# Kernel optimization log

Measured on AMD Instinct MI355X. Metric: run time of the kernel, lower is better.

## Reference

```python
import jax, jax.numpy as jnp
import numpy as np

B, S, F = 2048, 512, 64   # batch, seq_len, input_features
H = 32                    # LSTM_HIDDEN_SIZE
H1, H2 = 32, 16           # HIDDEN_SIZES
O = 3                     # output_features


def setup_inputs() -> dict:
    key = jax.random.key(0)
    ks = jax.random.split(key, 10)
    sc = lambda n: 1.0 / np.sqrt(n)
    x = jax.random.normal(ks[0], (B, S, F), dtype=jnp.float32)
    # LSTM kernels, gate order (i, f, g, o); input kernel has no bias (flax LSTMCell),
    # hidden kernel carries the bias.
    Wx = jax.random.normal(ks[1], (F, 4 * H), dtype=jnp.float32) * sc(F)
    Wh = jax.random.normal(ks[2], (H, 4 * H), dtype=jnp.float32) * sc(H)
    b = jnp.zeros((4 * H,), dtype=jnp.float32)
    # MLP head: 32 -> 32 -> 16 -> 3 with leaky_relu between hidden layers
    W1 = jax.random.normal(ks[3], (H, H1), dtype=jnp.float32) * sc(H)
    b1 = jnp.zeros((H1,), dtype=jnp.float32)
    W2 = jax.random.normal(ks[4], (H1, H2), dtype=jnp.float32) * sc(H1)
    b2 = jnp.zeros((H2,), dtype=jnp.float32)
    Wo = jax.random.normal(ks[5], (H2, O), dtype=jnp.float32) * sc(H2)
    bo = jnp.zeros((O,), dtype=jnp.float32)
    return {"x": x, "Wx": Wx, "Wh": Wh, "b": b,
            "W1": W1, "b1": b1, "W2": W2, "b2": b2, "Wo": Wo, "bo": bo}


def _lstm_last_hidden(x, Wx, Wh, b):
    # Precompute input-to-gate projections for all timesteps (same math,
    # hoists the [B,S,F]x[F,4H] GEMM out of the scan).
    bsz = x.shape[0]
    h_dim = Wh.shape[0]
    xg = jnp.einsum('bsf,fg->sbg', x, Wx)  # [S, B, 4H], time-major for scan

    def step(carry, xg_t):
        c, h = carry
        z = xg_t + h @ Wh + b               # [B, 4H]
        i, f, g, o = jnp.split(z, 4, axis=-1)
        i = jax.nn.sigmoid(i)
        f = jax.nn.sigmoid(f)
        g = jnp.tanh(g)
        o = jax.nn.sigmoid(o)
        c_new = f * c + i * g
        h_new = o * jnp.tanh(c_new)
        return (c_new, h_new), None

    c0 = jnp.zeros((bsz, h_dim), dtype=x.dtype)
    h0 = jnp.zeros((bsz, h_dim), dtype=x.dtype)
    (c_T, h_T), _ = jax.lax.scan(step, (c0, h0), xg)
    return h_T  # last hidden state, matches x[1][:, -1, :]


def reference(x, Wx, Wh, b, W1, b1, W2, b2, Wo, bo):
    h = _lstm_last_hidden(x, Wx, Wh, b)        # [B, H]
    a = jax.nn.leaky_relu(h @ W1 + b1)         # [B, 32]
    a = jax.nn.leaky_relu(a @ W2 + b2)         # [B, 16]
    return a @ Wo + bo                         # [B, O]
```

## Files before the change

kernel.cpp:

```cpp
#include <hip/hip_runtime.h>
#include <hip/hip_bf16.h>

#define S_  512
#define F_  64
#define H_  32
#define GQ  128
#define BT  8
#define NB  256

#define XS  72
#define HS  40
#define GS  33

#define L2E 1.4426950408889634f
#define CN2 (-2.8853900817779268f)

typedef __attribute__((ext_vector_type(8))) short bf16x8;
typedef __attribute__((ext_vector_type(4))) float f32x4;

__device__ __forceinline__ unsigned short bf16s(float f) {
    return __builtin_bit_cast(unsigned short, __float2bfloat16(f));
}
__device__ __forceinline__ unsigned bf16pk(float x, float y) {
    return (unsigned)bf16s(x) | ((unsigned)bf16s(y) << 16);
}
__device__ __forceinline__ float sigm2(float z) {
    return __builtin_amdgcn_rcpf(1.0f + __builtin_amdgcn_exp2f(-z));
}
__device__ __forceinline__ float tanh2(float c) {
    return 2.0f * __builtin_amdgcn_rcpf(1.0f + __builtin_amdgcn_exp2f(c * CN2)) - 1.0f;
}

#define MFMA(A, B, C) __builtin_amdgcn_mfma_f32_16x16x32_bf16(A, B, C, 0, 0, 0)

__global__ __launch_bounds__(512, 1)
void lstm_mfma_kernel(const float* __restrict__ x,  const float* __restrict__ Wx,
                      const float* __restrict__ Wh, const float* __restrict__ bg,
                      const float* __restrict__ W1, const float* __restrict__ b1,
                      const float* __restrict__ W2, const float* __restrict__ b2,
                      const float* __restrict__ Wo, const float* __restrict__ bo,
                      float* __restrict__ out)
{
    const int tid = threadIdx.x;
    const int w   = tid >> 6;
    const int L   = tid & 63;
    const int c16 = L & 15;
    const int kg  = L >> 4;
    const int bb  = blockIdx.x * BT;
    const int jj  = (w << 2) + kg;

    const int gcol = ((c16 & 3) << 5) + (w << 2) + (c16 >> 2);
    const float gsc = ((c16 & 3) == 2) ? (2.0f * L2E) : L2E;

    __shared__ __align__(16) unsigned short xh[4][16][XS];
    __shared__ __align__(16) unsigned short hh[2][16][HS];
    __shared__ float Hd[3][BT][GS];

    bf16x8 whh_, wx0h, wx1h;
#pragma unroll
    for (int i = 0; i < 8; ++i) {
        wx0h[i] = (short)bf16s(Wx[(kg * 8 + i) * GQ + gcol] * gsc);
        wx1h[i] = (short)bf16s(Wx[(32 + kg * 8 + i) * GQ + gcol] * gsc);
        whh_[i] = (short)bf16s(Wh[(kg * 8 + i) * GQ + gcol] * gsc);
    }
    f32x4 biasC;
#pragma unroll
    for (int r = 0; r < 4; ++r)
        biasC[r] = bg[r * 32 + jj] * ((r == 2) ? (2.0f * L2E) : L2E);

    for (int i = tid; i < 2 * 16 * (HS / 2); i += 512)
        ((unsigned*)&hh[0][0][0])[i] = 0u;

    const int srow = tid >> 5;
    const int sfp  = tid & 31;
    const int sdt  = srow >> 3;
    const float* xsrc = x + (size_t)(bb + (srow & 7)) * S_ * F_ + 2 * sfp;
    const float* xs2  = xsrc + (size_t)sdt * F_;
    {
#pragma unroll
        for (int tt = 0; tt < 2; ++tt) {
            float2 v = *(const float2*)(xs2 + (size_t)(2 * tt) * F_);
            *(unsigned*)&xh[tt][srow][2 * sfp] = bf16pk(v.x, v.y);
        }
    }
    float2 xvA = *(const float2*)(xs2 + (size_t)4 * F_);
    float2 xvB = *(const float2*)(xs2 + (size_t)6 * F_);
    __syncthreads();

    f32x4 xzA, xz1A, xzB, xz1B;
    {
        bf16x8 bxh0 = *(const bf16x8*)&xh[0][c16][kg * 8];
        bf16x8 bxh1 = *(const bf16x8*)&xh[0][c16][32 + kg * 8];
        f32x4 b0 = MFMA(wx0h, bxh0, biasC);
        xzA = MFMA(wx1h, bxh1, b0);
#pragma unroll
        for (int r = 0; r < 4; ++r) xz1A[r] = __shfl_xor(xzA[r], 8);
    }

    float cc = 0.0f;

#define DSTEP(TD, XZIN, XZ1IN, XZOUT, XZ1OUT, XV) {                            \
    const int td = (TD);                                                       \
         \
    *(unsigned*)&xh[(td + 2) & 3][srow][2 * sfp] = bf16pk(XV.x, XV.y);         \
    int tl = td + 4; if (tl > 255) tl = 255;                                   \
    XV = *(const float2*)(xs2 + (size_t)(2 * tl) * F_);                        \
    const int s1 = (td + 1) & 3;                                               \
           \
    bf16x8 bxh0 = *(const bf16x8*)&xh[s1][c16][kg * 8];                        \
    bf16x8 bhh1 = *(const bf16x8*)&hh[1][c16][kg * 8];                         \
    f32x4 part = MFMA(wx0h, bxh0, biasC);                                      \
    f32x4 z = MFMA(whh_, bhh1, XZIN);                                          \
    float iv = sigm2(z[0]), fv = sigm2(z[1]);                                  \
    float gv = 2.0f * sigm2(z[2]) - 1.0f, ov = sigm2(z[3]);                    \
    cc = fmaf(fv, cc, iv * gv);                                                \
    float hv = ov * tanh2(cc);                                                 \
    if (c16 < 8) hh[0][c16][jj] = bf16s(hv);                                   \
    __syncthreads();                                    \
                              \
    bf16x8 bxh1 = *(const bf16x8*)&xh[s1][c16][32 + kg * 8];                   \
    bf16x8 bhh0 = *(const bf16x8*)&hh[0][c16][kg * 8];                         \
    XZOUT = MFMA(wx1h, bxh1, part);                                            \
    _Pragma("unroll")                                                          \
    for (int r = 0; r < 4; ++r) XZ1OUT[r] = __shfl_xor(XZOUT[r], 8);           \
    z = MFMA(whh_, bhh0, XZ1IN);                                               \
    iv = sigm2(z[0]); fv = sigm2(z[1]);                                        \
    gv = 2.0f * sigm2(z[2]) - 1.0f; ov = sigm2(z[3]);                          \
    cc = fmaf(fv, cc, iv * gv);                                                \
    hv = ov * tanh2(cc);                                                       \
    if (c16 < 8) {                                                             \
        hh[1][c16][jj] = bf16s(hv);                                            \
        if (td == 255) Hd[0][c16][jj] = hv;                                    \
    }                                                                          \
    __syncthreads();                      \
}

    for (int qd = 0; qd < 128; ++qd) {
        DSTEP(2 * qd,     xzA, xz1A, xzB, xz1B, xvA)
        DSTEP(2 * qd + 1, xzB, xz1B, xzA, xz1A, xvB)
    }
#undef DSTEP

    __syncthreads();

    if (tid < 256) {
        int rb = tid >> 5, n = tid & 31;
        float a = b1[n];
#pragma unroll
        for (int k = 0; k < 32; ++k) a = fmaf(Hd[0][rb][k], W1[k * 32 + n], a);
        a = (a > 0.0f) ? a : 0.01f * a;
        Hd[1][rb][n] = a;
    }
    __syncthreads();
    if (tid < 128) {
        int rb = tid >> 4, n = tid & 15;
        float a = b2[n];
#pragma unroll
        for (int k = 0; k < 32; ++k) a = fmaf(Hd[1][rb][k], W2[k * 16 + n], a);
        a = (a > 0.0f) ? a : 0.01f * a;
        Hd[2][rb][n] = a;
    }
    __syncthreads();
    if (tid < 24) {
        int rb = tid / 3, n = tid - rb * 3;
        float a = bo[n];
#pragma unroll
        for (int k = 0; k < 16; ++k) a = fmaf(Hd[2][rb][k], Wo[k * 3 + n], a);
        out[(size_t)(bb + rb) * 3 + n] = a;
    }
}

extern "C" void kernel_launch(void* const* d_in, const int* in_sizes, int n_in,
                              void* d_out, int out_size, void* d_ws, size_t ws_size,
                              hipStream_t stream) {
    const float* x  = (const float*)d_in[0];
    const float* Wx = (const float*)d_in[1];
    const float* Wh = (const float*)d_in[2];
    const float* bg = (const float*)d_in[3];
    const float* W1 = (const float*)d_in[4];
    const float* b1 = (const float*)d_in[5];
    const float* W2 = (const float*)d_in[6];
    const float* b2 = (const float*)d_in[7];
    const float* Wo = (const float*)d_in[8];
    const float* bo = (const float*)d_in[9];
    float* out = (float*)d_out;

    hipLaunchKernelGGL(lstm_mfma_kernel, dim3(NB), dim3(512), 0, stream,
                       x, Wx, Wh, bg, W1, b1, W2, b2, Wo, bo, out);
}
```

Measured before the change: 139.4 us.

## Halve batch tile per block, run two blocks per CU, load x directly into registers

Each block now handles 4 batch rows instead of 8, doubling the block count, and launch bounds allow two blocks per CU so the latency-bound recurrence steps of two blocks can interleave. The LDS staging buffer for x is removed: each lane loads its own 8+8 float inputs straight from global memory a few steps ahead and converts them to bf16 in registers. This drops an LDS write/read round trip per step. In exchange, half the MFMA columns compute duplicate batch rows, global loads are redundant across lanes, and register pressure rises under the two-block occupancy target.

```diff
diff --git a/kernel.cpp b/kernel.cpp
--- a/kernel.cpp
+++ b/kernel.cpp
@@ -5,10 +5,9 @@
 #define F_  64
 #define H_  32
 #define GQ  128
-#define BT  8
-#define NB  256
-
-#define XS  72
+#define BT  4
+#define NB  512
+
 #define HS  40
 #define GS  33
 
@@ -24,6 +23,11 @@
 __device__ __forceinline__ unsigned bf16pk(float x, float y) {
     return (unsigned)bf16s(x) | ((unsigned)bf16s(y) << 16);
 }
+__device__ __forceinline__ bf16x8 mk8(float4 p, float4 q) {
+    uint4 t = { bf16pk(p.x, p.y), bf16pk(p.z, p.w),
+                bf16pk(q.x, q.y), bf16pk(q.z, q.w) };
+    return __builtin_bit_cast(bf16x8, t);
+}
 __device__ __forceinline__ float sigm2(float z) {
     return __builtin_amdgcn_rcpf(1.0f + __builtin_amdgcn_exp2f(-z));
 }
@@ -33,7 +37,7 @@
 
 #define MFMA(A, B, C) __builtin_amdgcn_mfma_f32_16x16x32_bf16(A, B, C, 0, 0, 0)
 
-__global__ __launch_bounds__(512, 1)
+__global__ __launch_bounds__(512, 2)
 void lstm_mfma_kernel(const float* __restrict__ x,  const float* __restrict__ Wx,
                       const float* __restrict__ Wh, const float* __restrict__ bg,
                       const float* __restrict__ W1, const float* __restrict__ b1,
@@ -52,7 +56,6 @@
     const int gcol = ((c16 & 3) << 5) + (w << 2) + (c16 >> 2);
     const float gsc = ((c16 & 3) == 2) ? (2.0f * L2E) : L2E;
 
-    __shared__ __align__(16) unsigned short xh[4][16][XS];
     __shared__ __align__(16) unsigned short hh[2][16][HS];
     __shared__ float Hd[3][BT][GS];
 
@@ -71,43 +74,52 @@
     for (int i = tid; i < 2 * 16 * (HS / 2); i += 512)
         ((unsigned*)&hh[0][0][0])[i] = 0u;
 
-    const int srow = tid >> 5;
-    const int sfp  = tid & 31;
-    const int sdt  = srow >> 3;
-    const float* xsrc = x + (size_t)(bb + (srow & 7)) * S_ * F_ + 2 * sfp;
-    const float* xs2  = xsrc + (size_t)sdt * F_;
-    {
-#pragma unroll
-        for (int tt = 0; tt < 2; ++tt) {
-            float2 v = *(const float2*)(xs2 + (size_t)(2 * tt) * F_);
-            *(unsigned*)&xh[tt][srow][2 * sfp] = bf16pk(v.x, v.y);
-        }
-    }
-    float2 xvA = *(const float2*)(xs2 + (size_t)4 * F_);
-    float2 xvB = *(const float2*)(xs2 + (size_t)6 * F_);
-    __syncthreads();
+    const int xbat = c16 & 3;
+    const int xdt  = c16 >> 3;
+    const float* xg = x + (size_t)(bb + xbat) * S_ * F_ + (size_t)xdt * F_;
+    const int f0 = kg * 8;
+
+    float4 aL0 = *(const float4*)(xg + (size_t)2 * F_ + f0);
+    float4 aL1 = *(const float4*)(xg + (size_t)2 * F_ + f0 + 4);
+    float4 aH0 = *(const float4*)(xg + (size_t)2 * F_ + 32 + f0);
+    float4 aH1 = *(const float4*)(xg + (size_t)2 * F_ + 32 + f0 + 4);
+    float4 bL0 = *(const float4*)(xg + (size_t)4 * F_ + f0);
+    float4 bL1 = *(const float4*)(xg + (size_t)4 * F_ + f0 + 4);
+    float4 bH0 = *(const float4*)(xg + (size_t)4 * F_ + 32 + f0);
+    float4 bH1 = *(const float4*)(xg + (size_t)4 * F_ + 32 + f0 + 4);
 
     f32x4 xzA, xz1A, xzB, xz1B;
     {
-        bf16x8 bxh0 = *(const bf16x8*)&xh[0][c16][kg * 8];
-        bf16x8 bxh1 = *(const bf16x8*)&xh[0][c16][32 + kg * 8];
+        float4 cL0 = *(const float4*)(xg + f0);
+        float4 cL1 = *(const float4*)(xg + f0 + 4);
+        float4 cH0 = *(const float4*)(xg + 32 + f0);
+        float4 cH1 = *(const float4*)(xg + 32 + f0 + 4);
+        bf16x8 bxh0 = mk8(cL0, cL1);
+        bf16x8 bxh1 = mk8(cH0, cH1);
         f32x4 b0 = MFMA(wx0h, bxh0, biasC);
         xzA = MFMA(wx1h, bxh1, b0);
 #pragma unroll
         for (int r = 0; r < 4; ++r) xz1A[r] = __shfl_xor(xzA[r], 8);
     }
+    __syncthreads();
 
     float cc = 0.0f;
 
-#define DSTEP(TD, XZIN, XZ1IN, XZOUT, XZ1OUT, XV) {                            \
+#define DSTEP(TD, PL0, PL1, PH0, PH1, XZIN, XZ1IN, XZOUT, XZ1OUT) {            \
     const int td = (TD);                                                       \
-         \
-    *(unsigned*)&xh[(td + 2) & 3][srow][2 * sfp] = bf16pk(XV.x, XV.y);         \
-    int tl = td + 4; if (tl > 255) tl = 255;                                   \
-    XV = *(const float2*)(xs2 + (size_t)(2 * tl) * F_);                        \
-    const int s1 = (td + 1) & 3;                                               \
+                    \
+    bf16x8 bxh0 = mk8(PL0, PL1);                                               \
+    bf16x8 bxh1 = mk8(PH0, PH1);                                               \
+                           \
+    {                                                                          \
+        int tl = td + 3; if (tl > 255) tl = 255;                               \
+        const float* pg = xg + (size_t)(2 * tl) * F_;                          \
+        PL0 = *(const float4*)(pg + f0);                                       \
+        PL1 = *(const float4*)(pg + f0 + 4);                                   \
+        PH0 = *(const float4*)(pg + 32 + f0);                                  \
+        PH1 = *(const float4*)(pg + 32 + f0 + 4);                              \
+    }                                                                          \
            \
-    bf16x8 bxh0 = *(const bf16x8*)&xh[s1][c16][kg * 8];                        \
     bf16x8 bhh1 = *(const bf16x8*)&hh[1][c16][kg * 8];                         \
     f32x4 part = MFMA(wx0h, bxh0, biasC);                                      \
     f32x4 z = MFMA(whh_, bhh1, XZIN);                                          \
@@ -118,7 +130,6 @@
     if (c16 < 8) hh[0][c16][jj] = bf16s(hv);                                   \
     __syncthreads();                                    \
                               \
-    bf16x8 bxh1 = *(const bf16x8*)&xh[s1][c16][32 + kg * 8];                   \
     bf16x8 bhh0 = *(const bf16x8*)&hh[0][c16][kg * 8];                         \
     XZOUT = MFMA(wx1h, bxh1, part);                                            \
     _Pragma("unroll")                                                          \
@@ -130,20 +141,20 @@
     hv = ov * tanh2(cc);                                                       \
     if (c16 < 8) {                                                             \
         hh[1][c16][jj] = bf16s(hv);                                            \
-        if (td == 255) Hd[0][c16][jj] = hv;                                    \
+        if (td == 255 && c16 < BT) Hd[0][c16][jj] = hv;                        \
     }                                                                          \
-    __syncthreads();                      \
+    __syncthreads();                                  \
 }
 
     for (int qd = 0; qd < 128; ++qd) {
-        DSTEP(2 * qd,     xzA, xz1A, xzB, xz1B, xvA)
-        DSTEP(2 * qd + 1, xzB, xz1B, xzA, xz1A, xvB)
+        DSTEP(2 * qd,     aL0, aL1, aH0, aH1, xzA, xz1A, xzB, xz1B)
+        DSTEP(2 * qd + 1, bL0, bL1, bH0, bH1, xzB, xz1B, xzA, xz1A)
     }
 #undef DSTEP
 
     __syncthreads();
 
-    if (tid < 256) {
+    if (tid < BT * 32) {
         int rb = tid >> 5, n = tid & 31;
         float a = b1[n];
 #pragma unroll
@@ -152,7 +163,7 @@
         Hd[1][rb][n] = a;
     }
     __syncthreads();
-    if (tid < 128) {
+    if (tid < BT * 16) {
         int rb = tid >> 4, n = tid & 15;
         float a = b2[n];
 #pragma unroll
@@ -161,7 +172,7 @@
         Hd[2][rb][n] = a;
     }
     __syncthreads();
-    if (tid < 24) {
+    if (tid < BT * 3) {
         int rb = tid / 3, n = tid - rb * 3;
         float a = bo[n];
 #pragma unroll
```

After: 460.6 us. 3.3x slower.
